# Kernel optimization log

Measured on AMD Instinct MI355X. Metric: run time of the kernel, lower is better.

The kernel has to match this reference:

```python
import jax, jax.numpy as jnp
import numpy as np

B, R, N, M, K = 4, 4, 4096, 64, 3
F_NUM = 512
KN = K * N


def _block(x, Ws, bs):
    """SO-Net PointResNet: 1x1 convs + ReLU; last layer sees concat(input, hidden)."""
    h = x
    for W, b in zip(Ws[:-1], bs[:-1]):
        h = jax.nn.relu(jnp.einsum('oc,bcn->bon', W, h) + b[None, :, None])
    h = jnp.concatenate([x, h], axis=1)
    return jax.nn.relu(jnp.einsum('oc,bcn->bon', Ws[-1], h) + bs[-1][None, :, None])


def _forward(x, intensity, node, node_knn_I, fpW, fpB, gpW, gpB):
    # --- som.query_topk: k nearest SOM nodes per point ---
    xd = jax.lax.stop_gradient(x)
    dist = jnp.sum((xd[:, :, :, None] - node[:, :, None, :]) ** 2, axis=1)      # B,N,M
    _, topk = jax.lax.top_k(-dist, K)                                           # B,N,K
    min_idx = topk.transpose(0, 2, 1).reshape(B, KN)                            # B,KN (k copies stacked)
    mask = jax.nn.one_hot(min_idx, M, dtype=jnp.float32)                        # B,KN,M
    mask_row_max = jnp.max(mask, axis=1) > 0                                    # B,M  node has >=1 point
    mask_row_sum = jnp.sum(mask, axis=1)                                        # B,M  points per node

    x_stack = jnp.tile(x, (1, 1, K))                                            # B,2,KN
    cluster_mean = jnp.einsum('bcn,bnm->bcm', jax.lax.stop_gradient(x_stack), mask) \
                   / (mask_row_sum[:, None, :] + 1e-5)                          # B,2,M (detached)

    # --- rotation group (2x2 rotations at angles 2*pi*r/R) ---
    theta = 2.0 * jnp.pi * jnp.arange(R, dtype=jnp.float32) / R
    c, s = jnp.cos(theta), jnp.sin(theta)
    rot = jnp.stack([jnp.stack([c, -s], -1), jnp.stack([s, c], -1)], -2)        # R,2,2

    x_rot = jnp.einsum('rij,bjn->brin', rot, x_stack)                           # B,R,2,KN
    node_rot = jnp.einsum('rij,bjm->brim', rot, cluster_mean)                   # B,R,2,M
    centers = jnp.take_along_axis(node_rot, min_idx[:, None, None, :], axis=3)  # B,R,2,KN
    x_dec = jax.lax.stop_gradient(x_rot - centers).reshape(B * R, 2, KN)

    # --- first PointResNet over all B*R rotation copies ---
    feat = _block(x_dec, fpW, fpB)                                              # BR,128,KN

    # --- index_max scatter-max per SOM cluster (value of argmax == segment max) ---
    seg = jnp.tile(min_idx[:, None, :], (1, R, 1)).reshape(B * R, KN)
    segmax = jax.vmap(lambda f, sgi: jax.ops.segment_max(f.T, sgi, num_segments=M).T)(feat, seg)
    rowmax = jnp.tile(mask_row_max[:, None, :], (1, R, 1)).reshape(B * R, M)
    pooled = jnp.where(rowmax[:, None, :], segmax, feat[:, :, 0:1])             # BR,128,M (empty -> gather idx 0)

    # --- final PointResNet over SOM nodes, then max over nodes and rotations ---
    g_in = jnp.concatenate([node_rot.reshape(B * R, 2, M), pooled], axis=1)     # BR,130,M
    out = _block(g_in, gpW, gpB)                                                # BR,F,M
    return out.reshape(B, R, F_NUM, M).max(axis=3).max(axis=1)                  # B,F


def setup_inputs() -> dict:
    key = jax.random.key(0)
    ks = jax.random.split(key, 24)
    d = {}
    d['x'] = jax.random.normal(ks[0], (B, 2, N), jnp.float32)
    d['intensity'] = jax.random.uniform(ks[1], (B, 1, N), jnp.float32)
    d['node'] = jax.random.normal(ks[2], (B, 2, M), jnp.float32)
    d['node_knn_I'] = jax.random.randint(ks[3], (B, M, 1), 0, M)
    dims_fp = [(64, 2), (64, 64), (128, 64), (128, 130)]      # PointResNet(2,[64,64,128,128])
    dims_gp = [(256, 130), (256, 256), (512, 256), (F_NUM, 642)]  # PointResNet(130,[256,256,512,F])
    i = 4
    for name, dims in (('fp', dims_fp), ('gp', dims_gp)):
        for j, (o, ci) in enumerate(dims):
            d[f'{name}_W{j}'] = jax.random.normal(ks[i], (o, ci), jnp.float32) / np.sqrt(ci).astype(np.float32)
            d[f'{name}_b{j}'] = jnp.zeros((o,), jnp.float32)
            i += 1
    return d


def reference(x, intensity, node, node_knn_I,
              fp_W0, fp_b0, fp_W1, fp_b1, fp_W2, fp_b2, fp_W3, fp_b3,
              gp_W0, gp_b0, gp_W1, gp_b1, gp_W2, gp_b2, gp_W3, gp_b3):
    return _forward(x, intensity, node, node_knn_I,
                    [fp_W0, fp_W1, fp_W2, fp_W3], [fp_b0, fp_b1, fp_b2, fp_b3],
                    [gp_W0, gp_W1, gp_W2, gp_W3], [gp_b0, gp_b1, gp_b2, gp_b3])
```

## Files before the change

kernel.cpp:

```cpp
#include <hip/hip_runtime.h>
#include <stdint.h>

#define BB 4
#define RR 4
#define NN 4096
#define MM 64
#define KK 3
#define KNN 12288
#define BRR 16
#define FF 512

typedef short bf16x8 __attribute__((ext_vector_type(8)));
typedef float f32x4 __attribute__((ext_vector_type(4)));

__device__ __forceinline__ float bf2f(unsigned int u) {
  union { unsigned int i; float f; } v; v.i = u << 16; return v.f;
}
__device__ __forceinline__ unsigned short f2bf(float f) {
  union { float f; unsigned int i; } v; v.f = f;
  unsigned int x = v.i;
  return (unsigned short)((x + 0x7fffu + ((x >> 16) & 1u)) >> 16);
}
__device__ __forceinline__ unsigned int cvtpk(float a, float b) {
  unsigned int r;
  asm("v_cvt_pk_bf16_f32 %0, %1, %2" : "=v"(r) : "v"(a), "v"(b));
  return r;
}
__device__ __forceinline__ float ldf(const void* p, long i, int isbf) {
  if (isbf) return bf2f(((const unsigned short*)p)[i]);
  return ((const float*)p)[i];
}
__device__ __forceinline__ int hsw(int col, int so) { return col * 72  + (so ^ (col & 24)); }
__device__ __forceinline__ int csw(int col, int so) { return col * 168 + (so ^ (col & 24)); }

struct WPtrs { const void* p[16]; };

__global__ __launch_bounds__(256) void k_front(
    const void* __restrict__ x, const void* __restrict__ node, WPtrs wp,
    int* __restrict__ flag, unsigned short* __restrict__ Wb,
    unsigned short* __restrict__ fW3p, float* __restrict__ Fb,
    int* __restrict__ idx, float* __restrict__ csum, int* __restrict__ blkcnt) {
  __shared__ int bad;
  __shared__ float nd[2][64];
  __shared__ float cs[192];
  int tid = threadIdx.x;
  if (tid == 0) bad = 0;
  __syncthreads();
  {
    const unsigned short* xs = (const unsigned short*)x;
    int cnt = 0;
    for (int i = tid; i < 1024; i += 256) {
      unsigned short u = xs[i * 2];
      int e = (u >> 7) & 0xFF;
      if (e >= 0x90 || (e > 0 && e <= 0x50)) ++cnt;
    }
    atomicAdd(&bad, cnt);
  }
  __syncthreads();
  int isbf = (bad < 100) ? 1 : 0;
  if (blockIdx.x == 0 && tid == 0) flag[0] = isbf;

  if (blockIdx.x < 2383) {
    const int e0=4096, e1=12288, e2=28928, e3=62208, e4=127744, e5=258816, e6=587520;
    int t = blockIdx.x * 256 + tid;
    if (t < e6) {
      int s, base;
      if      (t < e0) { s=0; base=0;  }
      else if (t < e1) { s=1; base=e0; }
      else if (t < e2) { s=2; base=e1; }
      else if (t < e3) { s=3; base=e2; }
      else if (t < e4) { s=4; base=e3; }
      else if (t < e5) { s=5; base=e4; }
      else             { s=6; base=e5; }
      int local = t - base;
      unsigned short u;
      if (isbf) u = ((const unsigned short*)wp.p[s])[local];
      else      u = f2bf(((const float*)wp.p[s])[local]);
      Wb[t] = u;
    } else if (t < 608000) {
      int l = t - e6;
      int o = l / 160, c = l - o * 160;
      unsigned short u = 0;
      if (c < 130) {
        long si = (long)o * 130 + c;
        if (isbf) u = ((const unsigned short*)wp.p[2])[si];
        else      u = f2bf(((const float*)wp.p[2])[si]);
      }
      fW3p[l] = u;
    } else if (t < 610048) {
      int l = t - 608000;
      const void* src; int off;
      if      (l < 128)  { src = wp.p[7];  off = 0;    }
      else if (l < 192)  { src = wp.p[8];  off = 128;  }
      else if (l < 256)  { src = wp.p[9];  off = 192;  }
      else if (l < 384)  { src = wp.p[10]; off = 256;  }
      else if (l < 512)  { src = wp.p[11]; off = 384;  }
      else if (l < 768)  { src = wp.p[12]; off = 512;  }
      else if (l < 1024) { src = wp.p[13]; off = 768;  }
      else if (l < 1536) { src = wp.p[14]; off = 1024; }
      else               { src = wp.p[15]; off = 1536; }
      Fb[l] = ldf(src, l - off, isbf);
    }
    return;
  }
  int bi = blockIdx.x - 2383;
  int b = bi >> 4;
  int n = ((bi & 15) << 8) + tid;
  if (tid < 128) nd[tid >> 6][tid & 63] = ldf(node, b * 128 + tid, isbf);
  if (tid < 192) cs[tid] = 0.f;
  __syncthreads();
  float x0 = ldf(x, b * 8192 + n, isbf);
  float x1 = ldf(x, b * 8192 + 4096 + n, isbf);
  float d0 = 1e30f, d1 = 1e30f, d2 = 1e30f;
  int m0 = 0, m1 = 0, m2 = 0;
#pragma unroll 8
  for (int m = 0; m < 64; ++m) {
    float dx = x0 - nd[0][m];
    float dy = x1 - nd[1][m];
    float d = __fmul_rn(dx, dx) + __fmul_rn(dy, dy);
    if (d < d0)      { d2=d1; m2=m1; d1=d0; m1=m0; d0=d; m0=m; }
    else if (d < d1) { d2=d1; m2=m1; d1=d;  m1=m; }
    else if (d < d2) { d2=d;  m2=m; }
  }
  long base = ((long)b * NN + n) * 3;
  idx[base] = m0; idx[base + 1] = m1; idx[base + 2] = m2;
  atomicAdd(&cs[m0*3+0], x0); atomicAdd(&cs[m0*3+1], x1); atomicAdd(&cs[m0*3+2], 1.f);
  atomicAdd(&cs[m1*3+0], x0); atomicAdd(&cs[m1*3+1], x1); atomicAdd(&cs[m1*3+2], 1.f);
  atomicAdd(&cs[m2*3+0], x0); atomicAdd(&cs[m2*3+1], x1); atomicAdd(&cs[m2*3+2], 1.f);
  __syncthreads();
  if (tid < 192) atomicAdd(&csum[b * 192 + tid], cs[tid]);
  if (tid < 64) blkcnt[bi * 64 + tid] = (int)cs[tid*3 + 2];
}

__global__ __launch_bounds__(256) void k_scatter2(
    const float* __restrict__ csum, const int* __restrict__ blkcnt,
    const int* __restrict__ idx, int* __restrict__ sorted,
    float* __restrict__ noderot, int* __restrict__ rowflag) {
  __shared__ int scnt[64];
  __shared__ int soff[64];
  __shared__ int lc[64];
  int tid = threadIdx.x;
  int blk = blockIdx.x;
  int b = blk >> 4, chunk = blk & 15;
  if (tid < 64) scnt[tid] = (int)csum[b*192 + tid*3 + 2];
  __syncthreads();
  if (tid < 64) {
    int m = tid, acc = 0;
    for (int mm = 0; mm < m; ++mm) acc += scnt[mm];
    for (int c = 0; c < chunk; ++c) acc += blkcnt[(b*16 + c)*64 + m];
    soff[m] = acc;
    lc[m] = 0;
    if (chunk == 0) {
      float s0 = csum[b*192 + m*3], s1 = csum[b*192 + m*3 + 1], cc = csum[b*192 + m*3 + 2];
      float mx = s0 / (cc + 1e-5f);
      float my = s1 / (cc + 1e-5f);
      rowflag[b*64 + m] = (cc > 0.f) ? 1 : 0;
      for (int r = 0; r < 4; ++r) {
        float th = 1.5707964f * (float)r;
        float cr = cosf(th), sr = sinf(th);
        noderot[((b*4 + r)*2 + 0)*64 + m] = cr*mx - sr*my;
        noderot[((b*4 + r)*2 + 1)*64 + m] = sr*mx + cr*my;
      }
    }
  }
  __syncthreads();
  int n = ((blk & 15) << 8) + tid;
#pragma unroll
  for (int kk = 0; kk < 3; ++kk) {
    int m = idx[((long)b * NN + n) * 3 + kk];
    int pos = atomicAdd(&lc[m], 1);
    sorted[b * KNN + soff[m] + pos] = (m << 12) | n;
  }
}

__global__ __launch_bounds__(256) void k_fused(
    const void* __restrict__ x, const int* __restrict__ sorted,
    const int* __restrict__ idx, const float* __restrict__ noderot,
    const int* __restrict__ flag, const unsigned short* __restrict__ Wb,
    const unsigned short* __restrict__ fW3p, const float* __restrict__ Fb,
    unsigned int* __restrict__ pooled, float* __restrict__ feat0) {
  __shared__ unsigned short Cs[64 * 168];
  __shared__ unsigned short Hs[64 * 72];
  __shared__ int mcol[64];
  const unsigned short* fW1 = Wb;
  const unsigned short* fW2 = Wb + 4096;
  int isbf = flag[0];
  int tid = threadIdx.x, lane = tid & 63, wv = tid >> 6;
  int quad = lane >> 4, lr = lane & 15;
  int br = blockIdx.y, b = br >> 2, r = br & 3;
  int o1 = wv * 16;
  if (tid < 64) {
    int e = sorted[b * KNN + blockIdx.x * 64 + tid];
    int m = e >> 12, n = e & 4095;
    int isz = (n == 0 && m == idx[(long)b * NN * 3]) ? 256 : 0;
    mcol[tid] = m | isz;
    float x0 = ldf(x, b*8192 + n, isbf), x1 = ldf(x, b*8192 + 4096 + n, isbf);
    float th = 1.5707964f * (float)r;
    float cr = cosf(th), sr = sinf(th);
    float xd0 = (cr*x0 - sr*x1) - noderot[(br*2 + 0)*64 + m];
    float xd1 = (sr*x0 + cr*x1) - noderot[(br*2 + 1)*64 + m];
    *(unsigned int*)&Cs[csw(tid, 0)] = cvtpk(xd0, xd1);
  }
  for (int z = tid; z < 960; z += 256) {
    int col = z / 15, l = 130 + (z - col * 15) * 2;
    *(unsigned int*)&Cs[csw(col, l)] = 0u;
  }
  __syncthreads();
  {
    int col = tid & 63, og = (tid >> 6) << 4;
    unsigned int xu = *(unsigned int*)&Cs[csw(col, 0)];
    float fx0 = bf2f(xu & 0xffff), fx1 = bf2f(xu >> 16);
    const float2* w2 = (const float2*)Fb;
    float hv[16];
#pragma unroll
    for (int j = 0; j < 16; ++j) {
      int o = og + j;
      float2 w = w2[o];
      float h = Fb[128 + o] + w.x * fx0 + w.y * fx1;
      hv[j] = fmaxf(h, 0.f);
    }
    union { bf16x8 v; unsigned int u[4]; } o8[2];
#pragma unroll
    for (int j = 0; j < 16; j += 2) o8[j >> 3].u[(j & 7) >> 1] = cvtpk(hv[j], hv[j+1]);
    *(bf16x8*)&Hs[hsw(col, og)]     = o8[0].v;
    *(bf16x8*)&Hs[hsw(col, og + 8)] = o8[1].v;
  }
  __syncthreads();
  {
    f32x4 acc[4];
#pragma unroll
    for (int nt = 0; nt < 4; ++nt)
      acc[nt] = (f32x4){Fb[192 + o1 + quad*4], Fb[192 + o1 + quad*4 + 1],
                        Fb[192 + o1 + quad*4 + 2], Fb[192 + o1 + quad*4 + 3]};
#pragma unroll
    for (int ks2 = 0; ks2 < 2; ++ks2) {
      bf16x8 a = *(const bf16x8*)(fW1 + (o1 + lr)*64 + ks2*32 + quad*8);
#pragma unroll
      for (int nt = 0; nt < 4; ++nt) {
        bf16x8 bf = *(bf16x8*)&Hs[hsw(nt*16 + lr, ks2*32 + quad*8)];
        acc[nt] = __builtin_amdgcn_mfma_f32_16x16x32_bf16(a, bf, acc[nt], 0, 0, 0);
      }
    }
    __syncthreads();
#pragma unroll
    for (int nt = 0; nt < 4; ++nt) {
      int col = nt*16 + lr;
      unsigned int lo = cvtpk(fmaxf(acc[nt][0], 0.f), fmaxf(acc[nt][1], 0.f));
      unsigned int hi = cvtpk(fmaxf(acc[nt][2], 0.f), fmaxf(acc[nt][3], 0.f));
      *(unsigned long long*)&Hs[hsw(col, o1 + quad*4)] =
          (unsigned long long)lo | ((unsigned long long)hi << 32);
    }
  }
  __syncthreads();
#pragma unroll
  for (int p2 = 0; p2 < 2; ++p2) {
    int o0 = p2*64 + o1;
    f32x4 acc[4];
#pragma unroll
    for (int nt = 0; nt < 4; ++nt)
      acc[nt] = (f32x4){Fb[256 + o0 + quad*4], Fb[256 + o0 + quad*4 + 1],
                        Fb[256 + o0 + quad*4 + 2], Fb[256 + o0 + quad*4 + 3]};
#pragma unroll
    for (int ks2 = 0; ks2 < 2; ++ks2) {
      bf16x8 a = *(const bf16x8*)(fW2 + (o0 + lr)*64 + ks2*32 + quad*8);
#pragma unroll
      for (int nt = 0; nt < 4; ++nt) {
        bf16x8 bf = *(bf16x8*)&Hs[hsw(nt*16 + lr, ks2*32 + quad*8)];
        acc[nt] = __builtin_amdgcn_mfma_f32_16x16x32_bf16(a, bf, acc[nt], 0, 0, 0);
      }
    }
#pragma unroll
    for (int nt = 0; nt < 4; ++nt) {
      int col = nt*16 + lr;
      int o = o0 + quad*4;
      unsigned int w0 = cvtpk(fmaxf(acc[nt][0], 0.f), fmaxf(acc[nt][1], 0.f));
      unsigned int w1 = cvtpk(fmaxf(acc[nt][2], 0.f), fmaxf(acc[nt][3], 0.f));
      *(unsigned int*)&Cs[csw(col, 2 + o)] = w0;
      *(unsigned int*)&Cs[csw(col, 4 + o)] = w1;
    }
  }
  __syncthreads();
  f32x4 acc3[2][4];
#pragma unroll
  for (int p3 = 0; p3 < 2; ++p3) {
    int o0 = p3*64 + o1;
#pragma unroll
    for (int nt = 0; nt < 4; ++nt)
      acc3[p3][nt] = (f32x4){Fb[384 + o0 + quad*4], Fb[384 + o0 + quad*4 + 1],
                             Fb[384 + o0 + quad*4 + 2], Fb[384 + o0 + quad*4 + 3]};
#pragma unroll
    for (int ks5 = 0; ks5 < 5; ++ks5) {
      bf16x8 a = *(const bf16x8*)(fW3p + (o0 + lr)*160 + ks5*32 + quad*8);
#pragma unroll
      for (int nt = 0; nt < 4; ++nt) {
        bf16x8 bf = *(bf16x8*)&Cs[csw(nt*16 + lr, ks5*32 + quad*8)];
        acc3[p3][nt] = __builtin_amdgcn_mfma_f32_16x16x32_bf16(a, bf, acc3[p3][nt], 0, 0, 0);
      }
    }
  }
  __syncthreads();
#pragma unroll
  for (int p3 = 0; p3 < 2; ++p3) {
    int o0 = p3*64 + o1;
#pragma unroll
    for (int nt = 0; nt < 4; ++nt) {
      int col = nt*16 + lr;
      unsigned int lo = cvtpk(fmaxf(acc3[p3][nt][0], 0.f), fmaxf(acc3[p3][nt][1], 0.f));
      unsigned int hi = cvtpk(fmaxf(acc3[p3][nt][2], 0.f), fmaxf(acc3[p3][nt][3], 0.f));
      *(unsigned long long*)&Cs[csw(col, o0 + quad*4)] =
          (unsigned long long)lo | ((unsigned long long)hi << 32);
    }
  }
  __syncthreads();
  {
    int opair = tid & 63, h = tid >> 6;
    int o0 = opair * 2;
    int c0 = h * 16;
    int curm = mcol[c0] & 255;
    unsigned int vlo = 0u, vhi = 0u;
    for (int c = c0; c < c0 + 16; ++c) {
      int mc = mcol[c];
      int mm = mc & 255;
      unsigned int u = *(unsigned int*)&Cs[csw(c, o0)];
      if (mm != curm) {
        atomicMax(&pooled[(((long)br*64 + curm) << 7) + o0],     vlo);
        atomicMax(&pooled[(((long)br*64 + curm) << 7) + o0 + 1], vhi);
        curm = mm; vlo = vhi = 0u;
      }
      vlo = max(vlo, u << 16);
      vhi = max(vhi, u & 0xffff0000u);
      if (mc & 256) {
        feat0[br*128 + o0]     = __uint_as_float(u << 16);
        feat0[br*128 + o0 + 1] = __uint_as_float(u & 0xffff0000u);
      }
    }
    atomicMax(&pooled[(((long)br*64 + curm) << 7) + o0],     vlo);
    atomicMax(&pooled[(((long)br*64 + curm) << 7) + o0 + 1], vhi);
  }
}

template<int OT, int KW, int KMAIN, bool REM2, int DSTR, int DOFF, int EPI>
__device__ __forceinline__ void gp_layer(
    const unsigned short* __restrict__ W, const float* __restrict__ bias,
    const unsigned short* Bs, int bstr, unsigned short* Ds,
    int wv, int quad, int lr, int b, unsigned int* __restrict__ outmax) {
  f32x4 acc[OT];
#pragma unroll
  for (int ot = 0; ot < OT; ++ot) {
    int o0 = (wv * OT + ot) * 16;
    acc[ot] = (f32x4){bias[o0 + quad*4], bias[o0 + quad*4 + 1],
                      bias[o0 + quad*4 + 2], bias[o0 + quad*4 + 3]};
  }
  const unsigned short* brow = Bs + lr * bstr;
  for (int ks = 0; ks < KMAIN; ks += 32) {
    bf16x8 bf = *(const bf16x8*)(brow + ks + quad*8);
    bf16x8 a[OT];
#pragma unroll
    for (int ot = 0; ot < OT; ++ot) {
      const unsigned short* arow = W + (long)((wv * OT + ot) * 16 + lr) * KW;
      if constexpr ((KW % 8) == 0) {
        a[ot] = *(const bf16x8*)(arow + ks + quad*8);
      } else {
        union { bf16x8 v; unsigned int u[4]; } au;
        const unsigned int* ap = (const unsigned int*)(arow + ks + quad*8);
        au.u[0] = ap[0]; au.u[1] = ap[1]; au.u[2] = ap[2]; au.u[3] = ap[3];
        a[ot] = au.v;
      }
    }
#pragma unroll
    for (int ot = 0; ot < OT; ++ot)
      acc[ot] = __builtin_amdgcn_mfma_f32_16x16x32_bf16(a[ot], bf, acc[ot], 0, 0, 0);
  }
  if constexpr (REM2) {
    unsigned int bu = *(const unsigned int*)(brow + KMAIN);
    float b0 = bf2f(bu & 0xffff), b1 = bf2f(bu >> 16);
#pragma unroll
    for (int ot = 0; ot < OT; ++ot) {
#pragma unroll
      for (int rr = 0; rr < 4; ++rr) {
        int o = (wv * OT + ot) * 16 + quad*4 + rr;
        unsigned int wu = *(const unsigned int*)(W + (long)o * KW + KMAIN);
        acc[ot][rr] += bf2f(wu & 0xffff) * b0 + bf2f(wu >> 16) * b1;
      }
    }
  }
#pragma unroll
  for (int ot = 0; ot < OT; ++ot) {
    int o0 = (wv * OT + ot) * 16;
    if constexpr (EPI == 0) {
      unsigned int lo = cvtpk(fmaxf(acc[ot][0], 0.f), fmaxf(acc[ot][1], 0.f));
      unsigned int hi = cvtpk(fmaxf(acc[ot][2], 0.f), fmaxf(acc[ot][3], 0.f));
      unsigned short* op = Ds + lr * DSTR + DOFF + o0 + quad*4;
      if constexpr ((DOFF & 3) == 0) {
        *(unsigned long long*)op = (unsigned long long)lo | ((unsigned long long)hi << 32);
      } else {
        *(unsigned int*)op       = lo;
        *(unsigned int*)(op + 2) = hi;
      }
    } else {
#pragma unroll
      for (int rr = 0; rr < 4; ++rr) {
        float v = fmaxf(acc[ot][rr], 0.f);
        v = fmaxf(v, __shfl_xor(v, 1, 64));
        v = fmaxf(v, __shfl_xor(v, 2, 64));
        v = fmaxf(v, __shfl_xor(v, 4, 64));
        v = fmaxf(v, __shfl_xor(v, 8, 64));
        if (lr == 0)
          atomicMax(&outmax[b * FF + o0 + quad*4 + rr], __float_as_uint(v));
      }
    }
  }
}

__global__ __launch_bounds__(1024) void k_gp(
    const unsigned int* __restrict__ pooled, const float* __restrict__ feat0,
    const int* __restrict__ rowflag, const float* __restrict__ noderot,
    const unsigned short* __restrict__ Wb, const float* __restrict__ Fb,
    unsigned int* __restrict__ outmax) {
  __shared__ unsigned short G3[16 * 648];
  __shared__ unsigned short H1[16 * 264];
  __shared__ unsigned short H2[16 * 264];
  const unsigned short* gW0 = Wb + 28928;
  const unsigned short* gW1 = Wb + 62208;
  const unsigned short* gW2 = Wb + 127744;
  const unsigned short* gW3 = Wb + 258816;
  int tid = threadIdx.x, lane = tid & 63, wv = tid >> 6;
  int quad = lane >> 4, lr = lane & 15;
  int c0 = blockIdx.x * 16;
  int br = c0 >> 6, b = br >> 2;
  {
    int j = tid >> 6, oq = (tid & 63) << 1;
    int col = c0 + j, m = col & 63;
    int fl = rowflag[b * 64 + m];
    float v0 = __uint_as_float(pooled[((long)col << 7) + oq]);
    float v1 = __uint_as_float(pooled[((long)col << 7) + oq + 1]);
    if (!fl) { v0 = feat0[br * 128 + oq]; v1 = feat0[br * 128 + oq + 1]; }
    *(unsigned int*)&G3[j * 648 + 2 + oq] = cvtpk(v0, v1);
    if (tid < 32) {
      int jj = tid >> 1, o = tid & 1;
      int mm = (c0 + jj) & 63;
      G3[jj * 648 + o] = f2bf(noderot[(br * 2 + o) * 64 + mm]);
    }
  }
  __syncthreads();
  gp_layer<1, 130, 128, true,  264, 0,   0>(gW0, Fb + 512,  G3, 648, H1, wv, quad, lr, b, outmax);
  __syncthreads();
  gp_layer<1, 256, 256, false, 264, 0,   0>(gW1, Fb + 768,  H1, 264, H2, wv, quad, lr, b, outmax);
  __syncthreads();
  gp_layer<2, 256, 256, false, 648, 130, 0>(gW2, Fb + 1024, H2, 264, G3, wv, quad, lr, b, outmax);
  __syncthreads();
  gp_layer<2, 642, 640, true,  0,   0,   1>(gW3, Fb + 1536, G3, 648, nullptr, wv, quad, lr, b, outmax);
}

__global__ __launch_bounds__(256) void k_out(
    const unsigned int* __restrict__ outmax, const int* __restrict__ flag,
    void* __restrict__ out) {
  int t = blockIdx.x * 256 + threadIdx.x;
  float v = __uint_as_float(outmax[t]);
  if (flag[0]) ((unsigned short*)out)[t] = f2bf(v);
  else         ((float*)out)[t] = v;
}

extern "C" void kernel_launch(void* const* d_in, const int* in_sizes, int n_in,
                              void* d_out, int out_size, void* d_ws, size_t ws_size,
                              hipStream_t stream) {
  const void* x    = d_in[0];
  const void* node = d_in[2];

  char* ws = (char*)d_ws;
  int*            flag    = (int*)(ws + 0);
  float*          csum    = (float*)(ws + 256);
  unsigned int*   outmax  = (unsigned int*)(ws + 3328);
  unsigned int*   pooled  = (unsigned int*)(ws + 11520);
  int*            idx     = (int*)(ws + 535808);
  int*            blkcnt  = (int*)(ws + 732416);
  float*          noderot = (float*)(ws + 766208);
  int*            rowflag = (int*)(ws + 774400);
  int*            sorted  = (int*)(ws + 775424);
  float*          feat0   = (float*)(ws + 972032);
  unsigned short* fW3p    = (unsigned short*)(ws + 980224);
  float*          Fb      = (float*)(ws + 1021184);
  unsigned short* Wb      = (unsigned short*)(ws + 3355904);

  hipMemsetAsync(ws, 0, 535808, stream);

  WPtrs wp;
  wp.p[0]=d_in[6];  wp.p[1]=d_in[8];  wp.p[2]=d_in[10];
  wp.p[3]=d_in[12]; wp.p[4]=d_in[14]; wp.p[5]=d_in[16]; wp.p[6]=d_in[18];
  wp.p[7]=d_in[4];
  wp.p[8]=d_in[5];  wp.p[9]=d_in[7];  wp.p[10]=d_in[9]; wp.p[11]=d_in[11];
  wp.p[12]=d_in[13]; wp.p[13]=d_in[15]; wp.p[14]=d_in[17]; wp.p[15]=d_in[19];

  k_front<<<2447, 256, 0, stream>>>(x, node, wp, flag, Wb, fW3p, Fb, idx, csum, blkcnt);
  k_scatter2<<<64, 256, 0, stream>>>(csum, blkcnt, idx, sorted, noderot, rowflag);
  k_fused<<<dim3(192, 16), 256, 0, stream>>>(x, sorted, idx, noderot, flag,
                                             Wb, fW3p, Fb, pooled, feat0);
  k_gp<<<64, 1024, 0, stream>>>(pooled, feat0, rowflag, noderot, Wb, Fb, outmax);
  k_out<<<8, 256, 0, stream>>>(outmax, flag, d_out);
}
```

Measured before the change: 198.7 us.

## Give each wave its own 16 columns to drop block-wide barriers in fused PointResNet

Changes the work split in the fused first-block kernel so each wave owns 16 point columns across all output channels, where before it owned 16 output channels across all 64 columns. Each wave then reads and writes only its own LDS columns, so every __syncthreads between layers can be removed and the B-operand fragments are loaded once and reused across output tiles. It also adds a minimum-4-blocks occupancy hint to launch_bounds. The cost is that each wave now streams the full weight matrices from global or cache instead of a slice, which multiplies weight traffic per wave, and the occupancy hint may force register spills.

```diff
diff --git a/kernel.cpp b/kernel.cpp
--- a/kernel.cpp
+++ b/kernel.cpp
@@ -173,7 +173,7 @@
   }
 }
 
-__global__ __launch_bounds__(256) void k_fused(
+__global__ __launch_bounds__(256, 4) void k_fused(
     const void* __restrict__ x, const int* __restrict__ sorted,
     const int* __restrict__ idx, const float* __restrict__ noderot,
     const int* __restrict__ flag, const unsigned short* __restrict__ Wb,
@@ -188,26 +188,24 @@
   int tid = threadIdx.x, lane = tid & 63, wv = tid >> 6;
   int quad = lane >> 4, lr = lane & 15;
   int br = blockIdx.y, b = br >> 2, r = br & 3;
-  int o1 = wv * 16;
-  if (tid < 64) {
-    int e = sorted[b * KNN + blockIdx.x * 64 + tid];
+  int cw = wv * 16;
+  if (lane < 16) {
+    int col = cw + lane;
+    int e = sorted[b * KNN + blockIdx.x * 64 + col];
     int m = e >> 12, n = e & 4095;
     int isz = (n == 0 && m == idx[(long)b * NN * 3]) ? 256 : 0;
-    mcol[tid] = m | isz;
+    mcol[col] = m | isz;
     float x0 = ldf(x, b*8192 + n, isbf), x1 = ldf(x, b*8192 + 4096 + n, isbf);
     float th = 1.5707964f * (float)r;
     float cr = cosf(th), sr = sinf(th);
     float xd0 = (cr*x0 - sr*x1) - noderot[(br*2 + 0)*64 + m];
     float xd1 = (sr*x0 + cr*x1) - noderot[(br*2 + 1)*64 + m];
-    *(unsigned int*)&Cs[csw(tid, 0)] = cvtpk(xd0, xd1);
-  }
-  for (int z = tid; z < 960; z += 256) {
-    int col = z / 15, l = 130 + (z - col * 15) * 2;
-    *(unsigned int*)&Cs[csw(col, l)] = 0u;
-  }
-  __syncthreads();
-  {
-    int col = tid & 63, og = (tid >> 6) << 4;
+    *(unsigned int*)&Cs[csw(col, 0)] = cvtpk(xd0, xd1);
+#pragma unroll
+    for (int z = 0; z < 15; ++z) *(unsigned int*)&Cs[csw(col, 130 + z*2)] = 0u;
+  }
+  {
+    int col = cw + lr, og = quad * 16;
     unsigned int xu = *(unsigned int*)&Cs[csw(col, 0)];
     float fx0 = bf2f(xu & 0xffff), fx1 = bf2f(xu >> 16);
     const float2* w2 = (const float2*)Fb;
@@ -225,97 +223,87 @@
     *(bf16x8*)&Hs[hsw(col, og)]     = o8[0].v;
     *(bf16x8*)&Hs[hsw(col, og + 8)] = o8[1].v;
   }
-  __syncthreads();
-  {
+  {
+    bf16x8 bfr[2];
+#pragma unroll
+    for (int ks2 = 0; ks2 < 2; ++ks2)
+      bfr[ks2] = *(bf16x8*)&Hs[hsw(cw + lr, ks2*32 + quad*8)];
     f32x4 acc[4];
 #pragma unroll
-    for (int nt = 0; nt < 4; ++nt)
-      acc[nt] = (f32x4){Fb[192 + o1 + quad*4], Fb[192 + o1 + quad*4 + 1],
-                        Fb[192 + o1 + quad*4 + 2], Fb[192 + o1 + quad*4 + 3]};
-#pragma unroll
-    for (int ks2 = 0; ks2 < 2; ++ks2) {
-      bf16x8 a = *(const bf16x8*)(fW1 + (o1 + lr)*64 + ks2*32 + quad*8);
-#pragma unroll
-      for (int nt = 0; nt < 4; ++nt) {
-        bf16x8 bf = *(bf16x8*)&Hs[hsw(nt*16 + lr, ks2*32 + quad*8)];
-        acc[nt] = __builtin_amdgcn_mfma_f32_16x16x32_bf16(a, bf, acc[nt], 0, 0, 0);
-      }
-    }
-    __syncthreads();
-#pragma unroll
-    for (int nt = 0; nt < 4; ++nt) {
-      int col = nt*16 + lr;
-      unsigned int lo = cvtpk(fmaxf(acc[nt][0], 0.f), fmaxf(acc[nt][1], 0.f));
-      unsigned int hi = cvtpk(fmaxf(acc[nt][2], 0.f), fmaxf(acc[nt][3], 0.f));
-      *(unsigned long long*)&Hs[hsw(col, o1 + quad*4)] =
+    for (int ot = 0; ot < 4; ++ot) {
+      int o0 = ot * 16;
+      acc[ot] = (f32x4){Fb[192 + o0 + quad*4], Fb[192 + o0 + quad*4 + 1],
+                        Fb[192 + o0 + quad*4 + 2], Fb[192 + o0 + quad*4 + 3]};
+#pragma unroll
+      for (int ks2 = 0; ks2 < 2; ++ks2) {
+        bf16x8 a = *(const bf16x8*)(fW1 + (o0 + lr)*64 + ks2*32 + quad*8);
+        acc[ot] = __builtin_amdgcn_mfma_f32_16x16x32_bf16(a, bfr[ks2], acc[ot], 0, 0, 0);
+      }
+    }
+#pragma unroll
+    for (int ot = 0; ot < 4; ++ot) {
+      int col = cw + lr;
+      unsigned int lo = cvtpk(fmaxf(acc[ot][0], 0.f), fmaxf(acc[ot][1], 0.f));
+      unsigned int hi = cvtpk(fmaxf(acc[ot][2], 0.f), fmaxf(acc[ot][3], 0.f));
+      *(unsigned long long*)&Hs[hsw(col, ot*16 + quad*4)] =
           (unsigned long long)lo | ((unsigned long long)hi << 32);
     }
   }
-  __syncthreads();
-#pragma unroll
-  for (int p2 = 0; p2 < 2; ++p2) {
-    int o0 = p2*64 + o1;
-    f32x4 acc[4];
-#pragma unroll
-    for (int nt = 0; nt < 4; ++nt)
-      acc[nt] = (f32x4){Fb[256 + o0 + quad*4], Fb[256 + o0 + quad*4 + 1],
-                        Fb[256 + o0 + quad*4 + 2], Fb[256 + o0 + quad*4 + 3]};
-#pragma unroll
-    for (int ks2 = 0; ks2 < 2; ++ks2) {
-      bf16x8 a = *(const bf16x8*)(fW2 + (o0 + lr)*64 + ks2*32 + quad*8);
-#pragma unroll
-      for (int nt = 0; nt < 4; ++nt) {
-        bf16x8 bf = *(bf16x8*)&Hs[hsw(nt*16 + lr, ks2*32 + quad*8)];
-        acc[nt] = __builtin_amdgcn_mfma_f32_16x16x32_bf16(a, bf, acc[nt], 0, 0, 0);
-      }
-    }
-#pragma unroll
-    for (int nt = 0; nt < 4; ++nt) {
-      int col = nt*16 + lr;
+  {
+    bf16x8 bfr[2];
+#pragma unroll
+    for (int ks2 = 0; ks2 < 2; ++ks2)
+      bfr[ks2] = *(bf16x8*)&Hs[hsw(cw + lr, ks2*32 + quad*8)];
+#pragma unroll
+    for (int ot = 0; ot < 8; ++ot) {
+      int o0 = ot * 16;
+      f32x4 acc = (f32x4){Fb[256 + o0 + quad*4], Fb[256 + o0 + quad*4 + 1],
+                          Fb[256 + o0 + quad*4 + 2], Fb[256 + o0 + quad*4 + 3]};
+#pragma unroll
+      for (int ks2 = 0; ks2 < 2; ++ks2) {
+        bf16x8 a = *(const bf16x8*)(fW2 + (o0 + lr)*64 + ks2*32 + quad*8);
+        acc = __builtin_amdgcn_mfma_f32_16x16x32_bf16(a, bfr[ks2], acc, 0, 0, 0);
+      }
+      int col = cw + lr;
       int o = o0 + quad*4;
-      unsigned int w0 = cvtpk(fmaxf(acc[nt][0], 0.f), fmaxf(acc[nt][1], 0.f));
-      unsigned int w1 = cvtpk(fmaxf(acc[nt][2], 0.f), fmaxf(acc[nt][3], 0.f));
-      *(unsigned int*)&Cs[csw(col, 2 + o)] = w0;
-      *(unsigned int*)&Cs[csw(col, 4 + o)] = w1;
-    }
-  }
-  __syncthreads();
+      *(unsigned int*)&Cs[csw(col, 2 + o)] = cvtpk(fmaxf(acc[0], 0.f), fmaxf(acc[1], 0.f));
+      *(unsigned int*)&Cs[csw(col, 4 + o)] = cvtpk(fmaxf(acc[2], 0.f), fmaxf(acc[3], 0.f));
+    }
+  }
   f32x4 acc3[2][4];
 #pragma unroll
   for (int p3 = 0; p3 < 2; ++p3) {
-    int o0 = p3*64 + o1;
-#pragma unroll
-    for (int nt = 0; nt < 4; ++nt)
-      acc3[p3][nt] = (f32x4){Fb[384 + o0 + quad*4], Fb[384 + o0 + quad*4 + 1],
+    bf16x8 bfr[5];
+#pragma unroll
+    for (int ks5 = 0; ks5 < 5; ++ks5)
+      bfr[ks5] = *(bf16x8*)&Cs[csw(cw + lr, ks5*32 + quad*8)];
+#pragma unroll
+    for (int ot = 0; ot < 4; ++ot) {
+      int o0 = p3*64 + ot*16;
+      acc3[p3][ot] = (f32x4){Fb[384 + o0 + quad*4], Fb[384 + o0 + quad*4 + 1],
                              Fb[384 + o0 + quad*4 + 2], Fb[384 + o0 + quad*4 + 3]};
 #pragma unroll
-    for (int ks5 = 0; ks5 < 5; ++ks5) {
-      bf16x8 a = *(const bf16x8*)(fW3p + (o0 + lr)*160 + ks5*32 + quad*8);
-#pragma unroll
-      for (int nt = 0; nt < 4; ++nt) {
-        bf16x8 bf = *(bf16x8*)&Cs[csw(nt*16 + lr, ks5*32 + quad*8)];
-        acc3[p3][nt] = __builtin_amdgcn_mfma_f32_16x16x32_bf16(a, bf, acc3[p3][nt], 0, 0, 0);
-      }
-    }
-  }
-  __syncthreads();
+      for (int ks5 = 0; ks5 < 5; ++ks5) {
+        bf16x8 a = *(const bf16x8*)(fW3p + (o0 + lr)*160 + ks5*32 + quad*8);
+        acc3[p3][ot] = __builtin_amdgcn_mfma_f32_16x16x32_bf16(a, bfr[ks5], acc3[p3][ot], 0, 0, 0);
+      }
+    }
+  }
 #pragma unroll
   for (int p3 = 0; p3 < 2; ++p3) {
-    int o0 = p3*64 + o1;
-#pragma unroll
-    for (int nt = 0; nt < 4; ++nt) {
-      int col = nt*16 + lr;
-      unsigned int lo = cvtpk(fmaxf(acc3[p3][nt][0], 0.f), fmaxf(acc3[p3][nt][1], 0.f));
-      unsigned int hi = cvtpk(fmaxf(acc3[p3][nt][2], 0.f), fmaxf(acc3[p3][nt][3], 0.f));
-      *(unsigned long long*)&Cs[csw(col, o0 + quad*4)] =
+#pragma unroll
+    for (int ot = 0; ot < 4; ++ot) {
+      int col = cw + lr;
+      int o = p3*64 + ot*16 + quad*4;
+      unsigned int lo = cvtpk(fmaxf(acc3[p3][ot][0], 0.f), fmaxf(acc3[p3][ot][1], 0.f));
+      unsigned int hi = cvtpk(fmaxf(acc3[p3][ot][2], 0.f), fmaxf(acc3[p3][ot][3], 0.f));
+      *(unsigned long long*)&Cs[csw(col, o)] =
           (unsigned long long)lo | ((unsigned long long)hi << 32);
     }
   }
-  __syncthreads();
-  {
-    int opair = tid & 63, h = tid >> 6;
-    int o0 = opair * 2;
-    int c0 = h * 16;
+  {
+    int o0 = lane * 2;
+    int c0 = cw;
     int curm = mcol[c0] & 255;
     unsigned int vlo = 0u, vhi = 0u;
     for (int c = c0; c < c0 + 16; ++c) {
```

Result: slower. 234.2 us (+17.9%).
